# Optimization experiments

Measured on AMD Instinct MI355X. Metric: run time of the kernel, lower is better.

## Reference

```python
import jax, jax.numpy as jnp
import numpy as np

TEMPERATURE = 128 ** 0.5  # sqrt(d_k)


def setup_inputs() -> dict:
    key = jax.random.key(0)
    k1, k2, k3 = jax.random.split(key, 3)
    NB, L, DK, DV = 1024, 2048, 128, 128
    q = jax.random.normal(k1, (NB, DK), dtype=jnp.float32)
    k = jax.random.normal(k2, (NB, L, DK), dtype=jnp.float32)
    v = jax.random.normal(k3, (NB, L, DV), dtype=jnp.float32)
    return {"q": q, "k": k, "v": v}


def reference(q, k, v):
    # attn[b, l] = <q[b], k[b, l]> / temperature
    scores = jnp.einsum('bd,bld->bl', q, k) / TEMPERATURE
    attn = jax.nn.softmax(scores, axis=1)  # softmax over l (dim=1)
    # output[b, d] = sum_l attn[b, l] * v[b, l, d]
    output = jnp.einsum('bl,bld->bd', attn, v)
    return (output, attn)
```

## Files before the change

### kernel.cpp

```cpp
#include <hip/hip_runtime.h>
#include <math.h>

#define NB 1024
#define L  2048
#define DK 128
#define DV 128

static constexpr float INV_TEMP = 0.088388347648318447f;

__global__ void mvsdpa_kernel(const float* __restrict__ q,
                              const float* __restrict__ k,
                              const float* __restrict__ v,
                              float* __restrict__ out,
                              float* __restrict__ attn)
{
    const int b    = blockIdx.x;
    const int tid  = threadIdx.x;
    const int wave = tid >> 6;
    const int lane = tid & 63;
    const int half = lane >> 5;
    const int l32  = lane & 31;

    __shared__ float s_scores[L];
    __shared__ float s_red[16];
    __shared__ float s_partial[8][DV];

    const float* qb = q + (size_t)b * DK;
    const float* kb = k + (size_t)b * (size_t)L * DK;
    const float* vb = v + (size_t)b * (size_t)L * DV;

    const float4 q4 = *reinterpret_cast<const float4*>(qb + l32 * 4);
    for (int l = wave * 2 + half; l < L; l += 16) {
        const float4 k4 = *reinterpret_cast<const float4*>(kb + (size_t)l * DK + l32 * 4);
        float acc = q4.x * k4.x + q4.y * k4.y + q4.z * k4.z + q4.w * k4.w;
        acc += __shfl_xor(acc, 1);
        acc += __shfl_xor(acc, 2);
        acc += __shfl_xor(acc, 4);
        acc += __shfl_xor(acc, 8);
        acc += __shfl_xor(acc, 16);
        if (l32 == 0) s_scores[l] = acc * INV_TEMP;
    }
    __syncthreads();

    float vals[4];
    float lmax = -INFINITY;
    #pragma unroll
    for (int i = 0; i < 4; ++i) {
        vals[i] = s_scores[tid + i * 512];
        lmax = fmaxf(lmax, vals[i]);
    }
    #pragma unroll
    for (int m = 1; m < 64; m <<= 1) lmax = fmaxf(lmax, __shfl_xor(lmax, m));
    if (lane == 0) s_red[wave] = lmax;
    __syncthreads();
    float bmax = s_red[0];
    #pragma unroll
    for (int w = 1; w < 8; ++w) bmax = fmaxf(bmax, s_red[w]);

    float lsum = 0.f;
    #pragma unroll
    for (int i = 0; i < 4; ++i) {
        vals[i] = __expf(vals[i] - bmax);
        lsum += vals[i];
    }
    #pragma unroll
    for (int m = 1; m < 64; m <<= 1) lsum += __shfl_xor(lsum, m);
    if (lane == 0) s_red[8 + wave] = lsum;
    __syncthreads();
    float bsum = 0.f;
    #pragma unroll
    for (int w = 0; w < 8; ++w) bsum += s_red[8 + w];
    const float inv = 1.0f / bsum;

    float* attn_b = attn + (size_t)b * L;
    #pragma unroll
    for (int i = 0; i < 4; ++i) {
        const float p = vals[i] * inv;
        s_scores[tid + i * 512] = p;
        attn_b[tid + i * 512] = p;
    }
    __syncthreads();

    float2 acc2 = make_float2(0.f, 0.f);
    for (int l = wave; l < L; l += 8) {
        const float  p  = s_scores[l];
        const float2 v2 = *reinterpret_cast<const float2*>(vb + (size_t)l * DV + lane * 2);
        acc2.x += p * v2.x;
        acc2.y += p * v2.y;
    }
    reinterpret_cast<float2*>(s_partial[wave])[lane] = acc2;
    __syncthreads();
    if (tid < DV) {
        float s = 0.f;
        #pragma unroll
        for (int w = 0; w < 8; ++w) s += s_partial[w][tid];
        out[(size_t)b * DV + tid] = s;
    }
}

extern "C" void kernel_launch(void* const* d_in, const int* in_sizes, int n_in,
                              void* d_out, int out_size, void* d_ws, size_t ws_size,
                              hipStream_t stream) {
    const float* q = (const float*)d_in[0];
    const float* k = (const float*)d_in[1];
    const float* v = (const float*)d_in[2];
    float* out  = (float*)d_out;
    float* attn = (float*)d_out + (size_t)NB * DV;
    mvsdpa_kernel<<<NB, 512, 0, stream>>>(q, k, v, out, attn);
}
```

Baseline: 370.3 us.

## Fuse QK, softmax and PV into single pass with online softmax per wave

```diff
diff --git a/kernel.cpp b/kernel.cpp
--- a/kernel.cpp
+++ b/kernel.cpp
@@ -8,11 +8,12 @@
 
 static constexpr float INV_TEMP = 0.088388347648318447f;
 
-__global__ void mvsdpa_kernel(const float* __restrict__ q,
-                              const float* __restrict__ k,
-                              const float* __restrict__ v,
-                              float* __restrict__ out,
-                              float* __restrict__ attn)
+__global__ __launch_bounds__(512, 8)
+void mvsdpa_kernel(const float* __restrict__ q,
+                   const float* __restrict__ k,
+                   const float* __restrict__ v,
+                   float* __restrict__ out,
+                   float* __restrict__ attn)
 {
     const int b    = blockIdx.x;
     const int tid  = threadIdx.x;
@@ -22,7 +23,8 @@
     const int l32  = lane & 31;
 
     __shared__ float s_scores[L];
-    __shared__ float s_red[16];
+    __shared__ float s_m[8];
+    __shared__ float s_s[8];
     __shared__ float s_partial[8][DV];
 
     const float* qb = q + (size_t)b * DK;
@@ -30,71 +32,68 @@
     const float* vb = v + (size_t)b * (size_t)L * DV;
 
     const float4 q4 = *reinterpret_cast<const float4*>(qb + l32 * 4);
-    for (int l = wave * 2 + half; l < L; l += 16) {
-        const float4 k4 = *reinterpret_cast<const float4*>(kb + (size_t)l * DK + l32 * 4);
-        float acc = q4.x * k4.x + q4.y * k4.y + q4.z * k4.z + q4.w * k4.w;
-        acc += __shfl_xor(acc, 1);
-        acc += __shfl_xor(acc, 2);
-        acc += __shfl_xor(acc, 4);
-        acc += __shfl_xor(acc, 8);
-        acc += __shfl_xor(acc, 16);
-        if (l32 == 0) s_scores[l] = acc * INV_TEMP;
+
+    const int l0 = wave * (L / 8);
+
+    float  m   = -INFINITY;
+    float  sum = 0.f;
+    float2 acc = make_float2(0.f, 0.f);
+
+    for (int i = 0; i < L / 8; i += 2) {
+        const int l = l0 + i;
+        const float4 k4 = *reinterpret_cast<const float4*>(kb + (size_t)(l + half) * DK + l32 * 4);
+        const float2 v0 = *reinterpret_cast<const float2*>(vb + (size_t)l       * DV + lane * 2);
+        const float2 v1 = *reinterpret_cast<const float2*>(vb + (size_t)(l + 1) * DV + lane * 2);
+
+        float d = q4.x * k4.x + q4.y * k4.y + q4.z * k4.z + q4.w * k4.w;
+        d += __shfl_xor(d, 1);
+        d += __shfl_xor(d, 2);
+        d += __shfl_xor(d, 4);
+        d += __shfl_xor(d, 8);
+        d += __shfl_xor(d, 16);
+        d *= INV_TEMP;
+        if (l32 == 0) s_scores[l + half] = d;
+
+        const float s0 = __shfl(d, 0);
+        const float s1 = __shfl(d, 32);
+
+        const float mn    = fmaxf(m, fmaxf(s0, s1));
+        const float scale = __expf(m - mn);
+        const float p0    = __expf(s0 - mn);
+        const float p1    = __expf(s1 - mn);
+        m   = mn;
+        sum = sum * scale + p0 + p1;
+        acc.x = acc.x * scale + p0 * v0.x + p1 * v1.x;
+        acc.y = acc.y * scale + p0 * v0.y + p1 * v1.y;
     }
+
+    if (lane == 0) { s_m[wave] = m; s_s[wave] = sum; }
     __syncthreads();
 
-    float vals[4];
-    float lmax = -INFINITY;
+    float gmax = s_m[0];
     #pragma unroll
-    for (int i = 0; i < 4; ++i) {
-        vals[i] = s_scores[tid + i * 512];
-        lmax = fmaxf(lmax, vals[i]);
-    }
+    for (int w = 1; w < 8; ++w) gmax = fmaxf(gmax, s_m[w]);
+    float gsum = 0.f;
     #pragma unroll
-    for (int m = 1; m < 64; m <<= 1) lmax = fmaxf(lmax, __shfl_xor(lmax, m));
-    if (lane == 0) s_red[wave] = lmax;
-    __syncthreads();
-    float bmax = s_red[0];
-    #pragma unroll
-    for (int w = 1; w < 8; ++w) bmax = fmaxf(bmax, s_red[w]);
-
-    float lsum = 0.f;
-    #pragma unroll
-    for (int i = 0; i < 4; ++i) {
-        vals[i] = __expf(vals[i] - bmax);
-        lsum += vals[i];
-    }
-    #pragma unroll
-    for (int m = 1; m < 64; m <<= 1) lsum += __shfl_xor(lsum, m);
-    if (lane == 0) s_red[8 + wave] = lsum;
-    __syncthreads();
-    float bsum = 0.f;
-    #pragma unroll
-    for (int w = 0; w < 8; ++w) bsum += s_red[8 + w];
-    const float inv = 1.0f / bsum;
+    for (int w = 0; w < 8; ++w) gsum += s_s[w] * __expf(s_m[w] - gmax);
+    const float inv = 1.0f / gsum;
 
     float* attn_b = attn + (size_t)b * L;
     #pragma unroll
     for (int i = 0; i < 4; ++i) {
-        const float p = vals[i] * inv;
-        s_scores[tid + i * 512] = p;
-        attn_b[tid + i * 512] = p;
+        const int idx = tid + i * 512;
+        attn_b[idx] = __expf(s_scores[idx] - gmax) * inv;
     }
-    __syncthreads();
 
-    float2 acc2 = make_float2(0.f, 0.f);
-    for (int l = wave; l < L; l += 8) {
-        const float  p  = s_scores[l];
-        const float2 v2 = *reinterpret_cast<const float2*>(vb + (size_t)l * DV + lane * 2);
-        acc2.x += p * v2.x;
-        acc2.y += p * v2.y;
-    }
-    reinterpret_cast<float2*>(s_partial[wave])[lane] = acc2;
+    const float wscale = __expf(m - gmax);
+    reinterpret_cast<float2*>(s_partial[wave])[lane] =
+        make_float2(acc.x * wscale, acc.y * wscale);
     __syncthreads();
     if (tid < DV) {
         float s = 0.f;
         #pragma unroll
         for (int w = 0; w < 8; ++w) s += s_partial[w][tid];
-        out[(size_t)b * DV + tid] = s;
+        out[(size_t)b * DV + tid] = s * inv;
     }
 }
 
```

Result: slower. 381.6 us (+3.1%).

## Unroll QK loop, widen V loads to float4, prefetch first V rows

Applied to the files above, without the earlier changes.

```diff
diff --git a/kernel.cpp b/kernel.cpp
--- a/kernel.cpp
+++ b/kernel.cpp
@@ -8,11 +8,12 @@
 
 static constexpr float INV_TEMP = 0.088388347648318447f;
 
-__global__ void mvsdpa_kernel(const float* __restrict__ q,
-                              const float* __restrict__ k,
-                              const float* __restrict__ v,
-                              float* __restrict__ out,
-                              float* __restrict__ attn)
+__global__ __launch_bounds__(512, 8)
+void mvsdpa_kernel(const float* __restrict__ q,
+                   const float* __restrict__ k,
+                   const float* __restrict__ v,
+                   float* __restrict__ out,
+                   float* __restrict__ attn)
 {
     const int b    = blockIdx.x;
     const int tid  = threadIdx.x;
@@ -23,77 +24,95 @@
 
     __shared__ float s_scores[L];
     __shared__ float s_red[16];
-    __shared__ float s_partial[8][DV];
+    __shared__ float s_partial[16][DV];
 
     const float* qb = q + (size_t)b * DK;
     const float* kb = k + (size_t)b * (size_t)L * DK;
     const float* vb = v + (size_t)b * (size_t)L * DV;
 
     const float4 q4 = *reinterpret_cast<const float4*>(qb + l32 * 4);
-    for (int l = wave * 2 + half; l < L; l += 16) {
-        const float4 k4 = *reinterpret_cast<const float4*>(kb + (size_t)l * DK + l32 * 4);
-        float acc = q4.x * k4.x + q4.y * k4.y + q4.z * k4.z + q4.w * k4.w;
-        acc += __shfl_xor(acc, 1);
-        acc += __shfl_xor(acc, 2);
-        acc += __shfl_xor(acc, 4);
-        acc += __shfl_xor(acc, 8);
-        acc += __shfl_xor(acc, 16);
-        if (l32 == 0) s_scores[l] = acc * INV_TEMP;
+
+    const int rbase = wave * 2 + half;
+
+    for (int i = 0; i < L / 32; ++i) {
+        const int r0 = i * 32 + rbase;
+        const int r1 = r0 + 16;
+        const float4 k40 = *reinterpret_cast<const float4*>(kb + (size_t)r0 * DK + l32 * 4);
+        const float4 k41 = *reinterpret_cast<const float4*>(kb + (size_t)r1 * DK + l32 * 4);
+        float d0 = q4.x * k40.x + q4.y * k40.y + q4.z * k40.z + q4.w * k40.w;
+        float d1 = q4.x * k41.x + q4.y * k41.y + q4.z * k41.z + q4.w * k41.w;
+        #pragma unroll
+        for (int m = 1; m < 32; m <<= 1) {
+            d0 += __shfl_xor(d0, m);
+            d1 += __shfl_xor(d1, m);
+        }
+        if (l32 == 0) {
+            s_scores[r0] = d0 * INV_TEMP;
+            s_scores[r1] = d1 * INV_TEMP;
+        }
     }
+
+    const float4 vp0 = *reinterpret_cast<const float4*>(vb + (size_t)rbase        * DV + l32 * 4);
+    const float4 vp1 = *reinterpret_cast<const float4*>(vb + (size_t)(rbase + 16) * DV + l32 * 4);
+
     __syncthreads();
 
-    float vals[4];
-    float lmax = -INFINITY;
-    #pragma unroll
-    for (int i = 0; i < 4; ++i) {
-        vals[i] = s_scores[tid + i * 512];
-        lmax = fmaxf(lmax, vals[i]);
-    }
+    float4 sv = *reinterpret_cast<const float4*>(&s_scores[tid * 4]);
+    float lmax = fmaxf(fmaxf(sv.x, sv.y), fmaxf(sv.z, sv.w));
     #pragma unroll
     for (int m = 1; m < 64; m <<= 1) lmax = fmaxf(lmax, __shfl_xor(lmax, m));
     if (lane == 0) s_red[wave] = lmax;
     __syncthreads();
-    float bmax = s_red[0];
+    float gmax = s_red[0];
     #pragma unroll
-    for (int w = 1; w < 8; ++w) bmax = fmaxf(bmax, s_red[w]);
+    for (int w = 1; w < 8; ++w) gmax = fmaxf(gmax, s_red[w]);
 
-    float lsum = 0.f;
-    #pragma unroll
-    for (int i = 0; i < 4; ++i) {
-        vals[i] = __expf(vals[i] - bmax);
-        lsum += vals[i];
-    }
+    sv.x = __expf(sv.x - gmax);
+    sv.y = __expf(sv.y - gmax);
+    sv.z = __expf(sv.z - gmax);
+    sv.w = __expf(sv.w - gmax);
+    float lsum = sv.x + sv.y + sv.z + sv.w;
     #pragma unroll
     for (int m = 1; m < 64; m <<= 1) lsum += __shfl_xor(lsum, m);
     if (lane == 0) s_red[8 + wave] = lsum;
     __syncthreads();
-    float bsum = 0.f;
+    float gsum = 0.f;
     #pragma unroll
-    for (int w = 0; w < 8; ++w) bsum += s_red[8 + w];
-    const float inv = 1.0f / bsum;
+    for (int w = 0; w < 8; ++w) gsum += s_red[8 + w];
+    const float inv = 1.0f / gsum;
 
-    float* attn_b = attn + (size_t)b * L;
-    #pragma unroll
-    for (int i = 0; i < 4; ++i) {
-        const float p = vals[i] * inv;
-        s_scores[tid + i * 512] = p;
-        attn_b[tid + i * 512] = p;
-    }
+    sv.x *= inv; sv.y *= inv; sv.z *= inv; sv.w *= inv;
+    *reinterpret_cast<float4*>(&s_scores[tid * 4]) = sv;
+    *reinterpret_cast<float4*>(attn + (size_t)b * L + tid * 4) = sv;
     __syncthreads();
 
-    float2 acc2 = make_float2(0.f, 0.f);
-    for (int l = wave; l < L; l += 8) {
-        const float  p  = s_scores[l];
-        const float2 v2 = *reinterpret_cast<const float2*>(vb + (size_t)l * DV + lane * 2);
-        acc2.x += p * v2.x;
-        acc2.y += p * v2.y;
+    float4 acc = make_float4(0.f, 0.f, 0.f, 0.f);
+    {
+        const float p0 = s_scores[rbase];
+        const float p1 = s_scores[rbase + 16];
+        acc.x = p0 * vp0.x + p1 * vp1.x;
+        acc.y = p0 * vp0.y + p1 * vp1.y;
+        acc.z = p0 * vp0.z + p1 * vp1.z;
+        acc.w = p0 * vp0.w + p1 * vp1.w;
     }
-    reinterpret_cast<float2*>(s_partial[wave])[lane] = acc2;
+    for (int i = 1; i < L / 32; ++i) {
+        const int r0 = i * 32 + rbase;
+        const int r1 = r0 + 16;
+        const float4 v0 = *reinterpret_cast<const float4*>(vb + (size_t)r0 * DV + l32 * 4);
+        const float4 v1 = *reinterpret_cast<const float4*>(vb + (size_t)r1 * DV + l32 * 4);
+        const float p0 = s_scores[r0];
+        const float p1 = s_scores[r1];
+        acc.x += p0 * v0.x + p1 * v1.x;
+        acc.y += p0 * v0.y + p1 * v1.y;
+        acc.z += p0 * v0.z + p1 * v1.z;
+        acc.w += p0 * v0.w + p1 * v1.w;
+    }
+    *reinterpret_cast<float4*>(&s_partial[wave * 2 + half][l32 * 4]) = acc;
     __syncthreads();
     if (tid < DV) {
         float s = 0.f;
         #pragma unroll
-        for (int w = 0; w < 8; ++w) s += s_partial[w][tid];
+        for (int w = 0; w < 16; ++w) s += s_partial[w][tid];
         out[(size_t)b * DV + tid] = s;
     }
 }
```

Result: faster. 355.3 us (-4.0%).
